# Optimization experiments

Measured on AMD Instinct MI355X. Metric: run time of the kernel, lower is better.

The kernel has to match this reference:

```python
import jax, jax.numpy as jnp
import numpy as np

WIN = 7          # window width (matches init win_size)
EPS = 1e-4       # Tikhonov regularization for the per-pixel normal equations
NF = 8           # features: [1, depth, albedo(3), normal(3)]


def _box_sum(x, win):
    # (windows are clipped at image borders, as in the CUDA kernel).
    ndim = x.ndim
    wdims = (1,) * (ndim - 2) + (win, win)
    return jax.lax.reduce_window(x, 0.0, jax.lax.add, wdims, (1,) * ndim, 'SAME')


def setup_inputs() -> dict:
    key = jax.random.key(0)
    k1, k2, k3, k4 = jax.random.split(key, 4)
    B, H, W = 1, 1024, 1024
    inp = jax.random.normal(k1, (B, 3, H, W), dtype=jnp.float32)
    depth = jax.random.uniform(k2, (B, 1, H, W), dtype=jnp.float32)
    albedo = jax.random.uniform(k3, (B, 3, H, W), dtype=jnp.float32)
    normal = jax.random.normal(k4, (B, 3, H, W), dtype=jnp.float32)
    normal = normal / (jnp.linalg.norm(normal, axis=1, keepdims=True) + 1e-6)
    return {"input": inp, "depth": depth, "albedo": albedo, "normal": normal}


def reference(input, depth, albedo, normal):
    B, C, H, W = input.shape
    ones = jnp.ones((B, 1, H, W), dtype=input.dtype)
    # Feature maps f: [B, 8, H, W] = [1, depth, albedo, normal]
    f = jnp.concatenate([ones, depth, albedo, normal], axis=1)

    # Per-pixel normal equations via box-filtered feature products.
    # AtA[b,i,j,h,w] = sum_{window} f_i * f_j   -> [B, 8, 8, H, W]
    AtA = _box_sum(f[:, :, None] * f[:, None], WIN)
    # AtY[b,i,c,h,w] = sum_{window} f_i * y_c   -> [B, 8, 3, H, W]
    AtY = _box_sum(f[:, :, None] * input[:, None], WIN)

    AtA = jnp.moveaxis(AtA, (1, 2), (3, 4))  # [B, H, W, 8, 8]
    AtY = jnp.moveaxis(AtY, (1, 2), (3, 4))  # [B, H, W, 8, 3]
    AtA = AtA + EPS * jnp.eye(NF, dtype=input.dtype)

    # Batched 8x8 solves, one per pixel.
    beta = jnp.linalg.solve(AtA, AtY)  # [B, H, W, 8, 3]

    # Evaluate fitted model at the center pixel's features.
    out = jnp.einsum('bhwfc,bfhw->bchw', beta, f)
    return out
```

## Files before the change

### kernel.cpp

```cpp
#include <hip/hip_runtime.h>
#include <math.h>

#define HH 1024
#define WW 1024
#define OUTW 58
#define RPB 4
#define WPB 4
#define OFF(i) ((i)*8 - (i)*((i)-1)/2)


template<int CTRL>
__device__ __forceinline__ float dpp0(float x) {
    return __int_as_float(
        __builtin_amdgcn_update_dpp(0, __float_as_int(x), CTRL, 0xf, 0xf, true));
}
__device__ __forceinline__ float wshr1(float x) { return dpp0<0x138>(x); }

__device__ __forceinline__ float frcp_fast(float s) {
    float r = __builtin_amdgcn_rcpf(s);
    return r * fmaf(-s, r, 2.0f);
}

__global__ __launch_bounds__(WPB * 64, 2) void ls_sep_kernel(
    const float* __restrict__ inp,
    const float* __restrict__ dep,
    const float* __restrict__ alb,
    const float* __restrict__ nrm,
    float* __restrict__ out)
{
    const int L  = threadIdx.x & 63;
    const int wv = threadIdx.x >> 6;
    const int HW = HH * WW;
    const int x  = OUTW * blockIdx.x - 3 + L;
    const int y0 = (RPB * WPB) * blockIdx.y + RPB * wv;
    const int px = x - 3;

    const int xc    = min(max(x, 0), WW - 1);
    const float xok = (x >= 0 && x < WW) ? 1.f : 0.f;

    float C[60];
    #pragma unroll
    for (int k = 0; k < 60; k++) C[k] = 0.f;

    auto load_row = [&](int yy, float fv[7], float yv[3]) -> float {
        const int yc = min(max(yy, 0), HH - 1);
        const float ok = (yy >= 0 && yy < HH) ? xok : 0.f;
        const int p = yc * WW + xc;
        fv[0] = dep[p];
        fv[1] = alb[p]; fv[2] = alb[p + HW]; fv[3] = alb[p + 2 * HW];
        fv[4] = nrm[p]; fv[5] = nrm[p + HW]; fv[6] = nrm[p + 2 * HW];
        yv[0] = inp[p]; yv[1] = inp[p + HW]; yv[2] = inp[p + 2 * HW];
        return ok;
    };
    auto acc_regs = [&](const float fv[7], const float yv[3], float s) {
        float f8[8];
        f8[0] = 1.f;
        #pragma unroll
        for (int i = 0; i < 7; i++) f8[i + 1] = fv[i];
        float fs[8];
        #pragma unroll
        for (int i = 0; i < 8; i++) fs[i] = f8[i] * s;
        int k = 0;
        #pragma unroll
        for (int i = 0; i < 8; i++)
            #pragma unroll
            for (int j = i; j < 8; j++) { C[k] = fmaf(fs[i], f8[j], C[k]); k++; }
        #pragma unroll
        for (int i = 0; i < 8; i++)
            #pragma unroll
            for (int c = 0; c < 3; c++)
                C[36 + i * 3 + c] = fmaf(fs[i], yv[c], C[36 + i * 3 + c]);
    };

    #pragma unroll 1
    for (int yy = y0 - 3; yy <= y0 + 3; yy++) {
        float fv[7], yv[3];
        const float ok = load_row(yy, fv, yv);
        acc_regs(fv, yv, ok);
    }

    const int idxm4 = ((L - 4) & 63) << 2;
    const int pxc = min(max(px, 0), WW - 1);
    const bool do_store = (L >= 6) && (px < WW);

    #pragma unroll 1
    for (int y = y0; y < y0 + RPB; y++) {
        float S[60];
        #pragma unroll
        for (int k = 0; k < 60; k++) {
            const float xv = C[k];
            const float w1 = wshr1(xv);
            const float t1 = xv + w1;
            const float w2 = wshr1(w1);
            const float t3 = t1 + w2;
            const float w3 = wshr1(w2);
            const float t2 = t3 + w3;
            const float pm = __int_as_float(
                __builtin_amdgcn_ds_bpermute(idxm4, __float_as_int(t3)));
            S[k] = t2 + pm;
        }

        float fE[7], yE[3], fL[7], yL[3];
        const float okE = load_row(y + 4, fE, yE);
        const float okL = load_row(y - 3, fL, yL);

        const int pc = y * WW + pxc;
        float cf[8];
        cf[0] = 1.f;
        cf[1] = dep[pc];
        cf[2] = alb[pc]; cf[3] = alb[pc + HW]; cf[4] = alb[pc + 2 * HW];
        cf[5] = nrm[pc]; cf[6] = nrm[pc + HW]; cf[7] = nrm[pc + 2 * HW];

        float W[36];
        #pragma unroll
        for (int k = 0; k < 36; k++) W[k] = S[k];
        #pragma unroll
        for (int i = 0; i < 8; i++) W[OFF(i)] += 1.0e-4f;

        float idv[8];
        #pragma unroll
        for (int i = 0; i < 8; i++) {
            #pragma unroll
            for (int k = 0; k < i; k++) {
                const float c = W[OFF(k) + i - k] * idv[k];
                #pragma unroll
                for (int j = i; j < 8; j++)
                    W[OFF(i) + j - i] = fmaf(-c, W[OFF(k) + j - k], W[OFF(i) + j - i]);
            }
            idv[i] = frcp_fast(W[OFF(i)]);
        }

        float vt[8];
        #pragma unroll
        for (int i = 0; i < 8; i++) {
            float s = cf[i];
            #pragma unroll
            for (int k = 0; k < i; k++)
                s = fmaf(-W[OFF(k) + i - k], vt[k], s);
            vt[i] = s * idv[i];
        }
        float w[8];
        #pragma unroll
        for (int i = 7; i >= 0; i--) {
            float t = 0.f;
            #pragma unroll
            for (int j = i + 1; j < 8; j++)
                t = fmaf(W[OFF(i) + j - i], w[j], t);
            w[i] = fmaf(-idv[i], t, vt[i]);
        }

        if (do_store) {
            const int p = y * WW + px;
            #pragma unroll
            for (int c = 0; c < 3; c++) {
                float r = 0.f;
                #pragma unroll
                for (int i = 0; i < 8; i++)
                    r = fmaf(w[i], S[36 + i * 3 + c], r);
                out[c * HW + p] = r;
            }
        }

        acc_regs(fE, yE, okE);
        acc_regs(fL, yL, -okL);
    }
}

extern "C" void kernel_launch(void* const* d_in, const int* in_sizes, int n_in,
                              void* d_out, int out_size, void* d_ws, size_t ws_size,
                              hipStream_t stream) {
    const float* inp = (const float*)d_in[0];
    const float* dep = (const float*)d_in[1];
    const float* alb = (const float*)d_in[2];
    const float* nrm = (const float*)d_in[3];
    float* out = (float*)d_out;
    dim3 grid((WW + OUTW - 1) / OUTW, HH / (RPB * WPB));
    ls_sep_kernel<<<grid, dim3(WPB * 64), 0, stream>>>(inp, dep, alb, nrm, out);
}
```

Baseline: 143.4 us.

## Pack normal-equation accumulators into float2 vectors for packed FMA and batched bpermute

Stores the symmetric 8x8 Gram matrix and the feature-target products as padded float2 pairs so that accumulation, the Cholesky-style elimination and the final dot product can use packed fp32 FMA. The horizontal box-sum is batched in groups so several ds_bpermute calls are in flight together. The vertical sliding-window update now runs before the solve in each row instead of after, which removes the separate S copy. The padded layout adds some redundant lanes, and the new schedule may change register pressure.

```diff
diff --git a/kernel.cpp b/kernel.cpp
--- a/kernel.cpp
+++ b/kernel.cpp
@@ -6,8 +6,13 @@
 #define OUTW 58
 #define RPB 4
 #define WPB 4
-#define OFF(i) ((i)*8 - (i)*((i)-1)/2)
-
+
+
+typedef float v2f __attribute__((ext_vector_type(2)));
+
+__device__ __constant__ const int RS_[8] = {0, 4, 8, 11, 14, 16, 18, 19};
+#define RS(i) ((i) == 0 ? 0 : (i) == 1 ? 4 : (i) == 2 ? 8 : (i) == 3 ? 11 : \
+               (i) == 4 ? 14 : (i) == 5 ? 16 : (i) == 6 ? 18 : 19)
 
 template<int CTRL>
 __device__ __forceinline__ float dpp0(float x) {
@@ -19,6 +24,33 @@
 __device__ __forceinline__ float frcp_fast(float s) {
     float r = __builtin_amdgcn_rcpf(s);
     return r * fmaf(-s, r, 2.0f);
+}
+
+template<int N>
+__device__ __forceinline__ void htapv(const v2f* src, v2f* dst, int idxm4) {
+    float t2a[2 * N];
+    int pma[2 * N];
+    #pragma unroll
+    for (int j = 0; j < N; j++) {
+        #pragma unroll
+        for (int h = 0; h < 2; h++) {
+            const float xv = h ? src[j].y : src[j].x;
+            const float w1 = wshr1(xv);
+            const float t1 = xv + w1;
+            const float w2 = wshr1(w1);
+            const float t3 = t1 + w2;
+            const float w3 = wshr1(w2);
+            t2a[2 * j + h] = t3 + w3;
+            pma[2 * j + h] = __builtin_amdgcn_ds_bpermute(idxm4, __float_as_int(t3));
+        }
+    }
+    #pragma unroll
+    for (int j = 0; j < N; j++) {
+        v2f d;
+        d.x = t2a[2 * j]     + __int_as_float(pma[2 * j]);
+        d.y = t2a[2 * j + 1] + __int_as_float(pma[2 * j + 1]);
+        dst[j] = d;
+    }
 }
 
 __global__ __launch_bounds__(WPB * 64, 2) void ls_sep_kernel(
@@ -38,46 +70,52 @@
     const int xc    = min(max(x, 0), WW - 1);
     const float xok = (x >= 0 && x < WW) ? 1.f : 0.f;
 
-    float C[60];
-    #pragma unroll
-    for (int k = 0; k < 60; k++) C[k] = 0.f;
-
-    auto load_row = [&](int yy, float fv[7], float yv[3]) -> float {
+    v2f CCA[20], CY[12];
+    #pragma unroll
+    for (int k = 0; k < 20; k++) CCA[k] = (v2f){0.f, 0.f};
+    #pragma unroll
+    for (int k = 0; k < 12; k++) CY[k] = (v2f){0.f, 0.f};
+
+    auto acc_vals = [&](const float f8[8], const float yv[3], float s) {
+        v2f F[4], Fs[4];
+        #pragma unroll
+        for (int p = 0; p < 4; p++) {
+            F[p].x = f8[2 * p]; F[p].y = f8[2 * p + 1];
+            Fs[p] = F[p] * (v2f){s, s};
+        }
+        #pragma unroll
+        for (int i = 0; i < 8; i++) {
+            const float fsi = (i & 1) ? Fs[i >> 1].y : Fs[i >> 1].x;
+            const v2f fb = (v2f){fsi, fsi};
+            #pragma unroll
+            for (int p = i >> 1; p < 4; p++)
+                CCA[RS(i) + p - (i >> 1)] =
+                    __builtin_elementwise_fma(fb, F[p], CCA[RS(i) + p - (i >> 1)]);
+        }
+        #pragma unroll
+        for (int c = 0; c < 3; c++) {
+            const v2f yb = (v2f){yv[c], yv[c]};
+            #pragma unroll
+            for (int p = 0; p < 4; p++)
+                CY[c * 4 + p] = __builtin_elementwise_fma(Fs[p], yb, CY[c * 4 + p]);
+        }
+    };
+
+    auto acc_row_g = [&](int yy, float sgn) {
         const int yc = min(max(yy, 0), HH - 1);
         const float ok = (yy >= 0 && yy < HH) ? xok : 0.f;
         const int p = yc * WW + xc;
-        fv[0] = dep[p];
-        fv[1] = alb[p]; fv[2] = alb[p + HW]; fv[3] = alb[p + 2 * HW];
-        fv[4] = nrm[p]; fv[5] = nrm[p + HW]; fv[6] = nrm[p + 2 * HW];
+        float f8[8], yv[3];
+        f8[0] = 1.f;
+        f8[1] = dep[p];
+        f8[2] = alb[p]; f8[3] = alb[p + HW]; f8[4] = alb[p + 2 * HW];
+        f8[5] = nrm[p]; f8[6] = nrm[p + HW]; f8[7] = nrm[p + 2 * HW];
         yv[0] = inp[p]; yv[1] = inp[p + HW]; yv[2] = inp[p + 2 * HW];
-        return ok;
+        acc_vals(f8, yv, sgn * ok);
     };
-    auto acc_regs = [&](const float fv[7], const float yv[3], float s) {
-        float f8[8];
-        f8[0] = 1.f;
-        #pragma unroll
-        for (int i = 0; i < 7; i++) f8[i + 1] = fv[i];
-        float fs[8];
-        #pragma unroll
-        for (int i = 0; i < 8; i++) fs[i] = f8[i] * s;
-        int k = 0;
-        #pragma unroll
-        for (int i = 0; i < 8; i++)
-            #pragma unroll
-            for (int j = i; j < 8; j++) { C[k] = fmaf(fs[i], f8[j], C[k]); k++; }
-        #pragma unroll
-        for (int i = 0; i < 8; i++)
-            #pragma unroll
-            for (int c = 0; c < 3; c++)
-                C[36 + i * 3 + c] = fmaf(fs[i], yv[c], C[36 + i * 3 + c]);
-    };
 
     #pragma unroll 1
-    for (int yy = y0 - 3; yy <= y0 + 3; yy++) {
-        float fv[7], yv[3];
-        const float ok = load_row(yy, fv, yv);
-        acc_regs(fv, yv, ok);
-    }
+    for (int yy = y0 - 4; yy < y0 + 3; yy++) acc_row_g(yy, 1.f);
 
     const int idxm4 = ((L - 4) & 63) << 2;
     const int pxc = min(max(px, 0), WW - 1);
@@ -85,24 +123,8 @@
 
     #pragma unroll 1
     for (int y = y0; y < y0 + RPB; y++) {
-        float S[60];
-        #pragma unroll
-        for (int k = 0; k < 60; k++) {
-            const float xv = C[k];
-            const float w1 = wshr1(xv);
-            const float t1 = xv + w1;
-            const float w2 = wshr1(w1);
-            const float t3 = t1 + w2;
-            const float w3 = wshr1(w2);
-            const float t2 = t3 + w3;
-            const float pm = __int_as_float(
-                __builtin_amdgcn_ds_bpermute(idxm4, __float_as_int(t3)));
-            S[k] = t2 + pm;
-        }
-
-        float fE[7], yE[3], fL[7], yL[3];
-        const float okE = load_row(y + 4, fE, yE);
-        const float okL = load_row(y - 3, fL, yL);
+        acc_row_g(y + 3, 1.f);
+        acc_row_g(y - 4, -1.f);
 
         const int pc = y * WW + pxc;
         float cf[8];
@@ -111,23 +133,33 @@
         cf[2] = alb[pc]; cf[3] = alb[pc + HW]; cf[4] = alb[pc + 2 * HW];
         cf[5] = nrm[pc]; cf[6] = nrm[pc + HW]; cf[7] = nrm[pc + 2 * HW];
 
-        float W[36];
-        #pragma unroll
-        for (int k = 0; k < 36; k++) W[k] = S[k];
-        #pragma unroll
-        for (int i = 0; i < 8; i++) W[OFF(i)] += 1.0e-4f;
+        v2f WA[20];
+        htapv<5>(&CCA[0],  &WA[0],  idxm4);
+        htapv<5>(&CCA[5],  &WA[5],  idxm4);
+        htapv<5>(&CCA[10], &WA[10], idxm4);
+        htapv<5>(&CCA[15], &WA[15], idxm4);
+        #pragma unroll
+        for (int i = 0; i < 8; i++) {
+            if (i & 1) WA[RS(i)].y += 1.0e-4f;
+            else       WA[RS(i)].x += 1.0e-4f;
+        }
+
+        #define GETEL(i, j) (((j) & 1) ? WA[RS(i) + ((j) >> 1) - ((i) >> 1)].y \
+                                       : WA[RS(i) + ((j) >> 1) - ((i) >> 1)].x)
 
         float idv[8];
         #pragma unroll
         for (int i = 0; i < 8; i++) {
             #pragma unroll
             for (int k = 0; k < i; k++) {
-                const float c = W[OFF(k) + i - k] * idv[k];
+                const float c = GETEL(k, i) * idv[k];
+                const v2f cb = (v2f){c, c};
                 #pragma unroll
-                for (int j = i; j < 8; j++)
-                    W[OFF(i) + j - i] = fmaf(-c, W[OFF(k) + j - k], W[OFF(i) + j - i]);
+                for (int p = i >> 1; p < 4; p++)
+                    WA[RS(i) + p - (i >> 1)] = __builtin_elementwise_fma(
+                        -cb, WA[RS(k) + p - (k >> 1)], WA[RS(i) + p - (i >> 1)]);
             }
-            idv[i] = frcp_fast(W[OFF(i)]);
+            idv[i] = frcp_fast(GETEL(i, i));
         }
 
         float vt[8];
@@ -136,7 +168,7 @@
             float s = cf[i];
             #pragma unroll
             for (int k = 0; k < i; k++)
-                s = fmaf(-W[OFF(k) + i - k], vt[k], s);
+                s = fmaf(-GETEL(k, i), vt[k], s);
             vt[i] = s * idv[i];
         }
         float w[8];
@@ -145,24 +177,33 @@
             float t = 0.f;
             #pragma unroll
             for (int j = i + 1; j < 8; j++)
-                t = fmaf(W[OFF(i) + j - i], w[j], t);
+                t = fmaf(GETEL(i, j), w[j], t);
             w[i] = fmaf(-idv[i], t, vt[i]);
+        }
+        #undef GETEL
+
+        v2f wp[4];
+        wp[0] = (v2f){w[0], w[1]}; wp[1] = (v2f){w[2], w[3]};
+        wp[2] = (v2f){w[4], w[5]}; wp[3] = (v2f){w[6], w[7]};
+        v2f CYt[12];
+        htapv<6>(&CY[0], &CYt[0], idxm4);
+        htapv<6>(&CY[6], &CYt[6], idxm4);
+        float r[3];
+        #pragma unroll
+        for (int c = 0; c < 3; c++) {
+            v2f a2 = (v2f){0.f, 0.f};
+            #pragma unroll
+            for (int p = 0; p < 4; p++)
+                a2 = __builtin_elementwise_fma(wp[p], CYt[c * 4 + p], a2);
+            r[c] = a2.x + a2.y;
         }
 
         if (do_store) {
             const int p = y * WW + px;
             #pragma unroll
-            for (int c = 0; c < 3; c++) {
-                float r = 0.f;
-                #pragma unroll
-                for (int i = 0; i < 8; i++)
-                    r = fmaf(w[i], S[36 + i * 3 + c], r);
-                out[c * HW + p] = r;
-            }
-        }
-
-        acc_regs(fE, yE, okE);
-        acc_regs(fL, yL, -okL);
+            for (int c = 0; c < 3; c++)
+                out[c * HW + p] = r[c];
+        }
     }
 }
 
```

Measured after the change: 137.0 us. 1.05x faster.
